# Kernel optimization log

Hardware: AMD Instinct MI355X
Metric: run time of the kernel (lower is better)

Reference implementation:

```python
import jax, jax.numpy as jnp
from jax import lax
import numpy as np

B, C, H, W = 4, 256, 64, 64
CQK = C // 8  # 32


def conv3x3(x, w, b):
    # x: [B,C_in,H,W], w: [C_out,C_in,3,3], b: [C_out]
    y = lax.conv_general_dilated(x, w, window_strides=(1, 1), padding='SAME',
                                 dimension_numbers=('NCHW', 'OIHW', 'NCHW'))
    return y + b[None, :, None, None]


def setup_inputs() -> dict:
    key = jax.random.key(0)
    ks = jax.random.split(key, 8)
    scale = 0.02
    return {
        'x': jax.random.normal(ks[0], (B, C, H, W), dtype=jnp.float32),
        'wq': jax.random.normal(ks[1], (CQK, C, 3, 3), dtype=jnp.float32) * scale,
        'bq': jax.random.normal(ks[2], (CQK,), dtype=jnp.float32) * scale,
        'wk': jax.random.normal(ks[3], (CQK, C, 3, 3), dtype=jnp.float32) * scale,
        'bk': jax.random.normal(ks[4], (CQK,), dtype=jnp.float32) * scale,
        'wv': jax.random.normal(ks[5], (C, C, 3, 3), dtype=jnp.float32) * scale,
        'bv': jax.random.normal(ks[6], (C,), dtype=jnp.float32) * scale,
        'gamma': jax.random.normal(ks[7], (1,), dtype=jnp.float32) * scale,
    }


def reference(x, wq, bq, wk, bk, wv, bv, gamma):
    b, c, h, w = x.shape
    n = h * w
    # Q: [B, N, C//8]  (permute(0,2,1) of the flattened conv output)
    q = conv3x3(x, wq, bq).reshape(b, -1, n).transpose(0, 2, 1)
    # K: [B, C//8, N]
    k = conv3x3(x, wk, bk).reshape(b, -1, n)
    # s: [B, N_q, N_k]
    s = jnp.einsum('bqd,bdk->bqk', q, k)
    # NOTE: original uses Softmax(dim=-2), i.e. over the QUERY axis
    attn_T = jax.nn.softmax(s, axis=-2)
    # V: [B, C, N]
    v = conv3x3(x, wv, bv).reshape(b, c, n)
    # o = bmm(V, attn_T): [B, C, N]
    o = jnp.einsum('bcq,bqk->bck', v, attn_T).reshape(b, c, h, w)
    return x + gamma * o
```

## Files before the change

### kernel.cpp

```cpp
#include <hip/hip_runtime.h>
#include <cstddef>

#define N_PIX 4096
#define HW 64
#define LOG2E 1.4426950408889634f
#define SHIFT2 28.8539008177793f

typedef __attribute__((ext_vector_type(8))) short bf16x8;
typedef __attribute__((ext_vector_type(4))) float f32x4;
typedef unsigned int u32;

static __device__ __forceinline__ unsigned short f2bf(float f) {
    union { float f; unsigned u; } v; v.f = f;
    unsigned r = v.u + 0x7fffu + ((v.u >> 16) & 1u);
    return (unsigned short)(r >> 16);
}
static __device__ __forceinline__ float bf2f(unsigned short s) {
    union { unsigned u; float f; } v; v.u = (unsigned)s << 16;
    return v.f;
}
static __device__ __forceinline__ unsigned pack_bf16_trunc(float lo, float hi) {
    union { float f; unsigned u; } a, b; a.f = hi; b.f = lo;
    return __builtin_amdgcn_perm(a.u, b.u, 0x07060302u);
}
static __device__ __forceinline__ void gll16(const void* g, void* l) {
    __builtin_amdgcn_global_load_lds(
        (const __attribute__((address_space(1))) u32*)g,
        (__attribute__((address_space(3))) u32*)l, 16, 0, 0);
}

__global__ __launch_bounds__(256) void prep_kernel(
    const float* __restrict__ x, unsigned short* __restrict__ xbf,
    const float* __restrict__ wq, const float* __restrict__ wk,
    const float* __restrict__ wv, unsigned short* __restrict__ wAll,
    unsigned short* __restrict__ zp)
{
    const int tid = threadIdx.x;
    if (blockIdx.z < 4) {
        __shared__ unsigned short Ts[64][72];
        const int px0 = blockIdx.x * 64, ci0 = blockIdx.y * 64, b = blockIdx.z;
        const float* xb = x + ((size_t)b * 256 + ci0) * N_PIX;

#pragma unroll
        for (int r = 0; r < 4; ++r) {
            int c = r * 16 + (tid >> 4);
            int p4 = (tid & 15) * 4;
            float4 v = *(const float4*)&xb[(size_t)c * N_PIX + px0 + p4];
            Ts[c][p4 + 0] = f2bf(v.x);
            Ts[c][p4 + 1] = f2bf(v.y);
            Ts[c][p4 + 2] = f2bf(v.z);
            Ts[c][p4 + 3] = f2bf(v.w);
        }
        __syncthreads();
#pragma unroll
        for (int r = 0; r < 2; ++r) {
            int id = tid * 2 + r;
            int p = id >> 3, c8 = (id & 7) * 8;
            ushort4 lo, hi;
            lo.x = Ts[c8 + 0][p]; lo.y = Ts[c8 + 1][p];
            lo.z = Ts[c8 + 2][p]; lo.w = Ts[c8 + 3][p];
            hi.x = Ts[c8 + 4][p]; hi.y = Ts[c8 + 5][p];
            hi.z = Ts[c8 + 6][p]; hi.w = Ts[c8 + 7][p];
            size_t off = ((size_t)b * N_PIX + px0 + p) * 256 + ci0 + c8;
            *(ushort4*)&xbf[off]     = lo;
            *(ushort4*)&xbf[off + 4] = hi;
        }
    } else {
        const int f = blockIdx.y * 64 + blockIdx.x;
#pragma unroll
        for (int base = 0; base < 2; ++base) {
            int gid = base * 65536 + f * 256 + tid;
            if (gid < 256) zp[gid] = 0;
            if (gid >= 72 * 320 * 4) continue;
            int part = gid & 3;
            int m = (gid >> 2) % 320;
            int kb = gid / 1280;
            int t = kb >> 3;
            int ci0 = (kb & 7) * 32 + part * 8;
            const float* src; int co; float sc = 1.f;
            if (m < 256)      { src = wv; co = m; }
            else if (m < 288) { src = wq; co = m - 256; sc = LOG2E; }
            else              { src = wk; co = m - 288; }
            ushort4 lo, hi;
            lo.x = f2bf(sc * src[((size_t)co * 256 + ci0 + 0) * 9 + t]);
            lo.y = f2bf(sc * src[((size_t)co * 256 + ci0 + 1) * 9 + t]);
            lo.z = f2bf(sc * src[((size_t)co * 256 + ci0 + 2) * 9 + t]);
            lo.w = f2bf(sc * src[((size_t)co * 256 + ci0 + 3) * 9 + t]);
            hi.x = f2bf(sc * src[((size_t)co * 256 + ci0 + 4) * 9 + t]);
            hi.y = f2bf(sc * src[((size_t)co * 256 + ci0 + 5) * 9 + t]);
            hi.z = f2bf(sc * src[((size_t)co * 256 + ci0 + 6) * 9 + t]);
            hi.w = f2bf(sc * src[((size_t)co * 256 + ci0 + 7) * 9 + t]);
            size_t off = ((size_t)kb * 320 + m) * 32 + part * 8;
            *(ushort4*)&wAll[off]     = lo;
            *(ushort4*)&wAll[off + 4] = hi;
        }
    }
}

__global__ __launch_bounds__(256, 2) void conv_gemm_v9(
    const unsigned short* __restrict__ xbf, const unsigned short* __restrict__ wAll,
    const float* __restrict__ bq, const float* __restrict__ bk,
    const float* __restrict__ bv, const unsigned short* __restrict__ zpage,
    unsigned short* __restrict__ vbf, unsigned short* __restrict__ qt,
    unsigned short* __restrict__ kt)
{
    __shared__ unsigned short Bl[3 * 7168];

    const int tid = threadIdx.x;
    const int w = tid >> 6, lane = tid & 63, quad = lane >> 4, l15 = lane & 15;
    const int y = blockIdx.x, rh = blockIdx.y, b = blockIdx.z;
    const int rg = w >> 1;
    const int pxh = w & 1;

    const unsigned short* xb = xbf + (size_t)b * N_PIX * 256;
    const unsigned short* aSrc = wAll + (size_t)rh * 160 * 32;

    auto stage = [&](int kb, int buf) {
        const int t_ = kb >> 3;
        const int ty = t_ / 3;
        const int dy = ty - 1, dx = t_ - ty * 3 - 1;
        const int gy = y + dy;
        const bool rowOK = ((unsigned)gy < 64u);
        const int ci0 = (kb & 7) * 32;
        const unsigned short* aS = aSrc + (size_t)kb * 10240;
        unsigned short* tile = &Bl[buf * 7168];
#pragma unroll
        for (int r = 0; r < 4; ++r) {
            const int c = r * 4 + w;
            if (r == 3 && w >= 2) continue;
            if (c < 10) {
                int o = c * 1024 + lane * 16;
                int u = o ^ (((o >> 7) & 7) << 4);
                gll16(aS + (u >> 1), tile + c * 512);
            } else {
                int o = (c - 10) * 1024 + lane * 16;
                int u = o ^ (((o >> 7) & 7) << 4);
                int px = u >> 6, k16 = (u >> 4) & 3;
                int gx = px + dx;
                const unsigned short* src =
                    (rowOK && (unsigned)gx < 64u)
                        ? xb + ((size_t)(gy * 64 + gx) * 256 + ci0 + k16 * 8)
                        : zpage;
                gll16(src, tile + 5120 + (c - 10) * 512);
            }
        }
    };

    f32x4 acc[5][2];
#pragma unroll
    for (int cb = 0; cb < 5; ++cb)
#pragma unroll
        for (int jb = 0; jb < 2; ++jb) acc[cb][jb] = (f32x4){0.f, 0.f, 0.f, 0.f};

    stage(0, 0);
    stage(1, 1);
    if (w < 2) asm volatile("s_waitcnt vmcnt(4)" ::: "memory");
    else       asm volatile("s_waitcnt vmcnt(3)" ::: "memory");
    __builtin_amdgcn_s_barrier();
    __builtin_amdgcn_sched_barrier(0);

#pragma unroll
    for (int kb = 0; kb < 72; ++kb) {
        const int buf = kb % 3;
        const int pb  = (kb + 2) % 3;
        const bool more2 = (kb + 2 < 72);
        const bool more1 = (kb + 1 < 72);
        if (more2) stage(kb + 2, pb);

        const int bb = buf * 7168;
        bf16x8 af[5], bfr[2];
#pragma unroll
        for (int cb = 0; cb < 5; ++cb) {
            int sr = rg * 80 + cb * 16 + l15;
            int u = sr * 64 + quad * 16;
            u ^= ((u >> 7) & 7) << 4;
            af[cb] = *(const bf16x8*)&Bl[bb + (u >> 1)];
        }
#pragma unroll
        for (int jb = 0; jb < 2; ++jb) {
            int px = pxh * 32 + jb * 16 + l15;
            int u = px * 64 + quad * 16;
            u ^= ((u >> 7) & 7) << 4;
            bfr[jb] = *(const bf16x8*)&Bl[bb + 5120 + (u >> 1)];
        }
        __builtin_amdgcn_s_setprio(1);
#pragma unroll
        for (int cb = 0; cb < 5; ++cb)
#pragma unroll
            for (int jb = 0; jb < 2; ++jb)
                acc[cb][jb] = __builtin_amdgcn_mfma_f32_16x16x32_bf16(
                    af[cb], bfr[jb], acc[cb][jb], 0, 0, 0);
        __builtin_amdgcn_s_setprio(0);

        if (more2) {
            if (w < 2) asm volatile("s_waitcnt vmcnt(4)" ::: "memory");
            else       asm volatile("s_waitcnt vmcnt(3)" ::: "memory");
        } else if (more1) {
            asm volatile("s_waitcnt vmcnt(0)" ::: "memory");
        }
        if (more1) {
            __builtin_amdgcn_s_barrier();
            __builtin_amdgcn_sched_barrier(0);
        }
    }

#pragma unroll
    for (int cb = 0; cb < 5; ++cb) {
        int cBase = rh * 160 + rg * 80 + cb * 16 + quad * 4;
#pragma unroll
        for (int r = 0; r < 4; ++r) {
            int c = cBase + r;
            if (c < 256) {
                float bias = bv[c];
#pragma unroll
                for (int jb = 0; jb < 2; ++jb) {
                    int px = y * 64 + pxh * 32 + jb * 16 + l15;
                    vbf[((size_t)b * 256 + c) * N_PIX + px] = f2bf(acc[cb][jb][r] + bias);
                }
            } else if (c < 288) {
                float bias = bq[c - 256] * LOG2E;
#pragma unroll
                for (int jb = 0; jb < 2; ++jb) {
                    int px = y * 64 + pxh * 32 + jb * 16 + l15;
                    qt[((size_t)b * N_PIX + px) * 32 + (c - 256)] = f2bf(acc[cb][jb][r] + bias);
                }
            } else {
                float bias = bk[c - 288];
#pragma unroll
                for (int jb = 0; jb < 2; ++jb) {
                    int px = y * 64 + pxh * 32 + jb * 16 + l15;
                    kt[((size_t)b * N_PIX + px) * 32 + (c - 288)] = f2bf(acc[cb][jb][r] + bias);
                }
            }
        }
    }
}

__global__ __launch_bounds__(256, 2) void fused_attn_mfma(
    const unsigned short* __restrict__ qt, const unsigned short* __restrict__ kt,
    const unsigned short* __restrict__ vbf,
    unsigned short* __restrict__ Abuf, float* __restrict__ lbuf, int iRange)
{
    const int tid  = threadIdx.x;
    const int w    = tid >> 6;
    const int lane = tid & 63;
    const int quad = lane >> 4;
    const int l15  = lane & 15;
    const int j0   = blockIdx.x * 128;
    const int b    = blockIdx.y;
    const int sp   = blockIdx.z;
    const int iBeg = sp * iRange;
    const int NI   = iRange / 64;

    const unsigned short* qtb = qt + (size_t)b * N_PIX * 32;
    const unsigned short* ktb = kt + (size_t)b * N_PIX * 32;
    const unsigned short* vb  = vbf + (size_t)b * 256 * N_PIX;

    __shared__ unsigned Pfrag[2][4096];
    __shared__ float lred[4][128];

    bf16x8 kf[8];
#pragma unroll
    for (int jb = 0; jb < 8; ++jb)
        kf[jb] = *(const bf16x8*)&ktb[((size_t)(j0 + jb * 16 + l15)) * 32 + quad * 8];

    f32x4 acc[4][8];
#pragma unroll
    for (int cb = 0; cb < 4; ++cb)
#pragma unroll
        for (int jb = 0; jb < 8; ++jb)
            acc[cb][jb] = (f32x4){0.f, 0.f, 0.f, 0.f};

    float lpart[8] = {0.f, 0.f, 0.f, 0.f, 0.f, 0.f, 0.f, 0.f};

    const int wFrag = w >> 1;
    const int wL    = ((w & 1) << 5) + ((quad >> 1) << 4) + l15;
    const int wEl2  = (quad & 1) << 1;

    bf16x8 va[2][4];

    auto s_phase = [&](bf16x8 qa, int buf) {
#pragma unroll
        for (int jb = 0; jb < 8; ++jb) {
            f32x4 s = __builtin_amdgcn_mfma_f32_16x16x32_bf16(
                qa, kf[jb], (f32x4){-SHIFT2, -SHIFT2, -SHIFT2, -SHIFT2}, 0, 0, 0);
            float p0 = __builtin_amdgcn_exp2f(s[0]);
            float p1 = __builtin_amdgcn_exp2f(s[1]);
            float p2 = __builtin_amdgcn_exp2f(s[2]);
            float p3 = __builtin_amdgcn_exp2f(s[3]);
            lpart[jb] += (p0 + p1) + (p2 + p3);
            unsigned u0 = pack_bf16_trunc(p0, p1);
            unsigned u1 = pack_bf16_trunc(p2, p3);
            unsigned base = (((jb << 1) + wFrag) * 64 + wL) * 4 + wEl2;
            Pfrag[buf][base]     = u0;
            Pfrag[buf][base + 1] = u1;
        }
    };

    auto load_qa = [&](int i0) {
        return *(const bf16x8*)&qtb[((size_t)(i0 + w * 16 + l15)) * 32 + quad * 8];
    };
    auto load_va = [&](int i0) {
#pragma unroll
        for (int ks = 0; ks < 2; ++ks)
#pragma unroll
            for (int cb = 0; cb < 4; ++cb)
                va[ks][cb] = *(const bf16x8*)&vb[((size_t)(w * 64 + cb * 16 + l15)) * N_PIX
                                                 + i0 + ks * 32 + quad * 8];
    };

    load_va(iBeg);
    s_phase(load_qa(iBeg), 0);

    for (int n = 0; n < NI; ++n) {
        __syncthreads();
        const bool hasN = (n + 1 < NI);
        const int inext = iBeg + (n + 1) * 64;
        bf16x8 qaN;
        if (hasN) qaN = load_qa(inext);

#pragma unroll
        for (int ks = 0; ks < 2; ++ks) {
            bf16x8 pb[8];
#pragma unroll
            for (int jb = 0; jb < 8; ++jb)
                pb[jb] = *(const bf16x8*)&Pfrag[n & 1][(((jb << 1) + ks) * 64 + lane) * 4];
#pragma unroll
            for (int cb = 0; cb < 4; ++cb)
#pragma unroll
                for (int jb = 0; jb < 8; ++jb)
                    acc[cb][jb] = __builtin_amdgcn_mfma_f32_16x16x32_bf16(
                        va[ks][cb], pb[jb], acc[cb][jb], 0, 0, 0);
        }

        if (hasN) {
            load_va(inext);
            s_phase(qaN, (n + 1) & 1);
        }
    }

#pragma unroll
    for (int jb = 0; jb < 8; ++jb) {
        float v = lpart[jb];
        v += __shfl_xor(v, 16, 64);
        v += __shfl_xor(v, 32, 64);
        lpart[jb] = v;
    }
    if (lane < 16) {
#pragma unroll
        for (int jb = 0; jb < 8; ++jb)
            lred[w][jb * 16 + l15] = lpart[jb];
    }
    __syncthreads();
    if (tid < 128) {
        float s = lred[0][tid] + lred[1][tid] + lred[2][tid] + lred[3][tid];
        lbuf[((size_t)sp * 4 + b) * N_PIX + j0 + tid] = s;
    }

    unsigned short* Ab = Abuf + ((size_t)sp * 4 + b) * 256 * N_PIX;
#pragma unroll
    for (int cb = 0; cb < 4; ++cb) {
        int c = w * 64 + cb * 16 + quad * 4;
#pragma unroll
        for (int jb = 0; jb < 8; ++jb) {
            int j = j0 + jb * 16 + l15;
#pragma unroll
            for (int r = 0; r < 4; ++r)
                Ab[(size_t)(c + r) * N_PIX + j] = f2bf(acc[cb][jb][r]);
        }
    }
}

__global__ __launch_bounds__(256) void combine_kernel(
    const unsigned short* __restrict__ A, const float* __restrict__ L,
    const float* __restrict__ x, const float* __restrict__ gamma,
    float* __restrict__ out, int split)
{
    const size_t CH = (size_t)4 * 256 * N_PIX;
    size_t flat = ((size_t)blockIdx.x * 256 + threadIdx.x) * 8;
    int j = (int)(flat & (N_PIX - 1));
    int b = (int)(flat >> 20);

    float a[8] = {0.f, 0.f, 0.f, 0.f, 0.f, 0.f, 0.f, 0.f};
    float l[8] = {0.f, 0.f, 0.f, 0.f, 0.f, 0.f, 0.f, 0.f};
    for (int s = 0; s < split; ++s) {
        ushort4 av0 = *(const ushort4*)&A[flat + (size_t)s * CH];
        ushort4 av1 = *(const ushort4*)&A[flat + (size_t)s * CH + 4];
        a[0] += bf2f(av0.x); a[1] += bf2f(av0.y); a[2] += bf2f(av0.z); a[3] += bf2f(av0.w);
        a[4] += bf2f(av1.x); a[5] += bf2f(av1.y); a[6] += bf2f(av1.z); a[7] += bf2f(av1.w);
        float4 l0 = *(const float4*)&L[((size_t)s * 4 + b) * N_PIX + j];
        float4 l1 = *(const float4*)&L[((size_t)s * 4 + b) * N_PIX + j + 4];
        l[0] += l0.x; l[1] += l0.y; l[2] += l0.z; l[3] += l0.w;
        l[4] += l1.x; l[5] += l1.y; l[6] += l1.z; l[7] += l1.w;
    }
    float g = gamma[0];
    float4 x0 = *(const float4*)&x[flat];
    float4 x1 = *(const float4*)&x[flat + 4];
    float4 o0, o1;
    o0.x = x0.x + g * a[0] / l[0];
    o0.y = x0.y + g * a[1] / l[1];
    o0.z = x0.z + g * a[2] / l[2];
    o0.w = x0.w + g * a[3] / l[3];
    o1.x = x1.x + g * a[4] / l[4];
    o1.y = x1.y + g * a[5] / l[5];
    o1.z = x1.z + g * a[6] / l[6];
    o1.w = x1.w + g * a[7] / l[7];
    *(float4*)&out[flat]     = o0;
    *(float4*)&out[flat + 4] = o1;
}

extern "C" void kernel_launch(void* const* d_in, const int* in_sizes, int n_in,
                              void* d_out, int out_size, void* d_ws, size_t ws_size,
                              hipStream_t stream)
{
    const float* x     = (const float*)d_in[0];
    const float* wq    = (const float*)d_in[1];
    const float* bq    = (const float*)d_in[2];
    const float* wk    = (const float*)d_in[3];
    const float* bk    = (const float*)d_in[4];
    const float* wv    = (const float*)d_in[5];
    const float* bv    = (const float*)d_in[6];
    const float* gamma = (const float*)d_in[7];
    float* out = (float*)d_out;

    const size_t szQTel  = (size_t)4 * N_PIX * 32;
    const size_t szVBFel = (size_t)4 * 256 * N_PIX;
    const size_t szXBFel = (size_t)4 * N_PIX * 256;
    const size_t szWel   = (size_t)72 * 320 * 32;
    const size_t fixedB  = (2 * szQTel + szVBFel + szXBFel + szWel + 256) * 2;

    int split = 4;
    while (split > 1) {
        size_t need = fixedB
                    + (size_t)split * 4 * 256 * N_PIX * 2
                    + (size_t)split * 4 * N_PIX * 4;
        if (need <= ws_size) break;
        split >>= 1;
    }

    unsigned short* Abuf = (unsigned short*)d_ws;
    float* lbuf = (float*)(Abuf + (size_t)split * 4 * 256 * N_PIX);
    unsigned short* qt    = (unsigned short*)(lbuf + (size_t)split * 4 * N_PIX);
    unsigned short* kt    = qt + szQTel;
    unsigned short* vbf   = kt + szQTel;
    unsigned short* xbf   = vbf + szVBFel;
    unsigned short* wAll  = xbf + szXBFel;
    unsigned short* zpage = wAll + szWel;

    prep_kernel<<<dim3(N_PIX / 64, 4, 5), 256, 0, stream>>>(
        x, xbf, wq, wk, wv, wAll, zpage);

    conv_gemm_v9<<<dim3(HW, 2, 4), 256, 0, stream>>>(
        xbf, wAll, bq, bk, bv, zpage, vbf, qt, kt);

    fused_attn_mfma<<<dim3(N_PIX / 128, 4, split), 256, 0, stream>>>(
        qt, kt, vbf, Abuf, lbuf, N_PIX / split);

    combine_kernel<<<dim3((4 * 256 * N_PIX) / (256 * 8)), 256, 0, stream>>>(
        Abuf, lbuf, x, gamma, out, split);
}
```

Baseline: 175.8 us.

## Stage V tiles into swizzled LDS via async global-to-LDS loads with manual waitcnts

Each wave no longer loads its V fragments straight from global memory into registers. Instead it prefetches them into a per-wave, double-buffered, XOR-swizzled LDS region using 16-byte direct global-to-LDS loads, then reads the MFMA A operands back from LDS. Hand-placed vmcnt/lgkmcnt waits and raw s_barrier calls replace __syncthreads so the next tile's V loads overlap the current MFMA work. This frees registers and hides global latency. In exchange it adds LDS traffic and fragile hand-counted waitcnts, which could reduce occupancy through the larger LDS footprint.

```diff
diff --git a/kernel.cpp b/kernel.cpp
--- a/kernel.cpp
+++ b/kernel.cpp
@@ -254,9 +254,10 @@
 
     const unsigned short* qtb = qt + (size_t)b * N_PIX * 32;
     const unsigned short* ktb = kt + (size_t)b * N_PIX * 32;
-    const unsigned short* vb  = vbf + (size_t)b * 256 * N_PIX;
+    const unsigned short* vb  = vbf + ((size_t)b * 256 + w * 64) * N_PIX;
 
     __shared__ unsigned Pfrag[2][4096];
+    __shared__ unsigned short Vl[4][2][2048];
     __shared__ float lred[4][128];
 
     bf16x8 kf[8];
@@ -277,7 +278,24 @@
     const int wL    = ((w & 1) << 5) + ((quad >> 1) << 4) + l15;
     const int wEl2  = (quad & 1) << 1;
 
-    bf16x8 va[2][4];
+    auto stageV = [&](int c0, int vbuf) {
+#pragma unroll
+        for (int r = 0; r < 4; ++r) {
+            int o = r * 1024 + lane * 16;
+            int u = o ^ (((o >> 7) & 7) << 4);
+            const unsigned short* src =
+                vb + (size_t)(u >> 6) * N_PIX + c0 + ((u & 63) >> 1);
+            gll16(src, &Vl[w][vbuf][r * 512]);
+        }
+    };
+    auto readVa = [&](int vbuf, bf16x8 (&va)[4]) {
+#pragma unroll
+        for (int cb = 0; cb < 4; ++cb) {
+            int o = (cb * 16 + l15) * 64 + quad * 16;
+            int u = o ^ (((o >> 7) & 7) << 4);
+            va[cb] = *(const bf16x8*)&Vl[w][vbuf][u >> 1];
+        }
+    };
 
     auto s_phase = [&](bf16x8 qa, int buf) {
 #pragma unroll
@@ -300,43 +318,60 @@
     auto load_qa = [&](int i0) {
         return *(const bf16x8*)&qtb[((size_t)(i0 + w * 16 + l15)) * 32 + quad * 8];
     };
-    auto load_va = [&](int i0) {
-#pragma unroll
-        for (int ks = 0; ks < 2; ++ks)
-#pragma unroll
-            for (int cb = 0; cb < 4; ++cb)
-                va[ks][cb] = *(const bf16x8*)&vb[((size_t)(w * 64 + cb * 16 + l15)) * N_PIX
-                                                 + i0 + ks * 32 + quad * 8];
-    };
-
-    load_va(iBeg);
+
+    stageV(iBeg, 0);
+    stageV(iBeg + 32, 1);
     s_phase(load_qa(iBeg), 0);
+    asm volatile("s_waitcnt lgkmcnt(0)" ::: "memory");
+    __builtin_amdgcn_s_barrier();
+    __builtin_amdgcn_sched_barrier(0);
 
     for (int n = 0; n < NI; ++n) {
-        __syncthreads();
         const bool hasN = (n + 1 < NI);
         const int inext = iBeg + (n + 1) * 64;
         bf16x8 qaN;
         if (hasN) qaN = load_qa(inext);
 
-#pragma unroll
-        for (int ks = 0; ks < 2; ++ks) {
-            bf16x8 pb[8];
+        bf16x8 pb[8], va[4];
+
+#pragma unroll
+        for (int jb = 0; jb < 8; ++jb)
+            pb[jb] = *(const bf16x8*)&Pfrag[n & 1][((jb << 1) * 64 + lane) * 4];
+        if (hasN) asm volatile("s_waitcnt vmcnt(5)" ::: "memory");
+        else      asm volatile("s_waitcnt vmcnt(4)" ::: "memory");
+        __builtin_amdgcn_sched_barrier(0);
+        readVa(0, va);
+        asm volatile("s_waitcnt lgkmcnt(0)" ::: "memory");
+        __builtin_amdgcn_sched_barrier(0);
+        if (hasN) stageV(inext, 0);
+#pragma unroll
+        for (int cb = 0; cb < 4; ++cb)
 #pragma unroll
             for (int jb = 0; jb < 8; ++jb)
-                pb[jb] = *(const bf16x8*)&Pfrag[n & 1][(((jb << 1) + ks) * 64 + lane) * 4];
-#pragma unroll
-            for (int cb = 0; cb < 4; ++cb)
-#pragma unroll
-                for (int jb = 0; jb < 8; ++jb)
-                    acc[cb][jb] = __builtin_amdgcn_mfma_f32_16x16x32_bf16(
-                        va[ks][cb], pb[jb], acc[cb][jb], 0, 0, 0);
-        }
-
-        if (hasN) {
-            load_va(inext);
-            s_phase(qaN, (n + 1) & 1);
-        }
+                acc[cb][jb] = __builtin_amdgcn_mfma_f32_16x16x32_bf16(
+                    va[cb], pb[jb], acc[cb][jb], 0, 0, 0);
+
+#pragma unroll
+        for (int jb = 0; jb < 8; ++jb)
+            pb[jb] = *(const bf16x8*)&Pfrag[n & 1][(((jb << 1) + 1) * 64 + lane) * 4];
+        if (hasN) asm volatile("s_waitcnt vmcnt(5)" ::: "memory");
+        else      asm volatile("s_waitcnt vmcnt(0)" ::: "memory");
+        __builtin_amdgcn_sched_barrier(0);
+        readVa(1, va);
+        asm volatile("s_waitcnt lgkmcnt(0)" ::: "memory");
+        __builtin_amdgcn_sched_barrier(0);
+        if (hasN) stageV(inext + 32, 1);
+#pragma unroll
+        for (int cb = 0; cb < 4; ++cb)
+#pragma unroll
+            for (int jb = 0; jb < 8; ++jb)
+                acc[cb][jb] = __builtin_amdgcn_mfma_f32_16x16x32_bf16(
+                    va[cb], pb[jb], acc[cb][jb], 0, 0, 0);
+
+        if (hasN) s_phase(qaN, (n + 1) & 1);
+        asm volatile("s_waitcnt lgkmcnt(0)" ::: "memory");
+        __builtin_amdgcn_s_barrier();
+        __builtin_amdgcn_sched_barrier(0);
     }
 
 #pragma unroll
```

New measurement: 175.4 us (median of 2 runs). About the same (-0.2%).
